# Kernel tuning notes

Hardware: AMD Instinct MI355X
Metric: run time of the kernel (lower is better)

The kernel has to match this reference:

```python
import jax, jax.numpy as jnp
import numpy as np

N = 200000
E = 600000
H = 128
OUT = 256
NUM_TYPES = 300
B = 128


def setup_inputs() -> dict:
    key = jax.random.key(0)
    ks = jax.random.split(key, 12)
    x = jax.random.randint(ks[0], (N,), 0, NUM_TYPES)
    edge_index = jax.random.randint(ks[1], (2, E), 0, N)
    batch = jnp.sort(jax.random.randint(ks[2], (N,), 0, B))
    s = 1.0 / np.sqrt(H)
    emb = jax.random.normal(ks[3], (NUM_TYPES, H), jnp.float32)
    W0 = jax.random.uniform(ks[4], (H, H), jnp.float32, -s, s)
    b0 = jax.random.uniform(ks[5], (H,), jnp.float32, -s, s)
    W1 = jax.random.uniform(ks[6], (H, H), jnp.float32, -s, s)
    b1 = jax.random.uniform(ks[7], (H,), jnp.float32, -s, s)
    Wo = jax.random.uniform(ks[8], (H, OUT), jnp.float32, -s, s)
    bo = jax.random.uniform(ks[9], (OUT,), jnp.float32, -s, s)
    gamma = jnp.ones((OUT,), jnp.float32)
    beta = jnp.zeros((OUT,), jnp.float32)
    return {"x": x, "edge_index": edge_index, "batch": batch, "batch_size": B,
            "emb": emb, "W0": W0, "b0": b0, "W1": W1, "b1": b1,
            "Wo": Wo, "bo": bo, "gamma": gamma, "beta": beta}


def gcn_layer(h, full_src, full_dst, W, b, n):
    # gather messages, scatter-add to destinations (bidirectional edges pre-built)
    msg = h[full_src]                                   # [2E, H]
    agg = jax.ops.segment_sum(msg, full_dst, num_segments=n)
    deg = jax.ops.segment_sum(jnp.ones((full_src.shape[0],), h.dtype),
                              full_dst, num_segments=n)
    deg = jnp.sqrt(jnp.clip(deg, 1.0))[:, None]
    out = agg / deg
    out = out @ W + b
    out = out + h
    return jax.nn.gelu(out, approximate=False)  # torch nn.GELU default is exact


def reference(x, edge_index, batch, batch_size, emb, W0, b0, W1, b1, Wo, bo, gamma, beta):
    n = x.shape[0]
    h = emb[x]                                          # [N, H] embedding gather
    src, dst = edge_index[0], edge_index[1]
    full_src = jnp.concatenate([src, dst])
    full_dst = jnp.concatenate([dst, src])
    h = gcn_layer(h, full_src, full_dst, W0, b0, n)
    h = gcn_layer(h, full_src, full_dst, W1, b1, n)
    # segment-mean pooling per graph
    gsum = jax.ops.segment_sum(h, batch, num_segments=batch_size)
    cnt = jax.ops.segment_sum(jnp.ones((n,), h.dtype), batch, num_segments=batch_size)
    gfeat = gsum / jnp.clip(cnt, 1.0)[:, None]
    out = gfeat @ Wo + bo
    mu = jnp.mean(out, axis=-1, keepdims=True)
    var = jnp.var(out, axis=-1, keepdims=True)
    out = (out - mu) * jax.lax.rsqrt(var + 1e-5) * gamma + beta
    return out
```

## Files before the change

### kernel.cpp

```cpp
#include <hip/hip_runtime.h>
#include <hip/hip_bf16.h>
#include <hip/hip_fp8.h>
#include <math.h>

#define H 128
#define OUTD 256
#define ASTRIDE 40
#define NODE_MASK 0x3FFFF

typedef unsigned short ushort_t;
typedef unsigned int uint_t;
typedef unsigned char uchar_t;
typedef __attribute__((ext_vector_type(8))) short short8;
typedef __attribute__((ext_vector_type(4))) float f32x4;
typedef __attribute__((ext_vector_type(2))) float f32x2;

__device__ __forceinline__ float bf2f(uint_t u){
    union { uint_t i; float f; } v; v.i = u << 16; return v.f;
}
__device__ __forceinline__ uint_t f2bf(float f){
    __hip_bfloat16 b = __float2bfloat16(f);
    union { __hip_bfloat16 b; ushort_t u; } v; v.b = b; return (uint_t)v.u;
}
__device__ __forceinline__ float fp8tof(uint_t u){
    __hip_fp8_e4m3 t; t.__x = (__hip_fp8_storage_t)u; return (float)t;
}
__device__ __forceinline__ uint_t ftofp8(float f){
    __hip_fp8_e4m3 t(f); return (uint_t)t.__x;
}
__device__ __forceinline__ uint_t pk2fp8(float a, float b){
#if __has_builtin(__builtin_amdgcn_cvt_pk_fp8_f32)
    return (uint_t)__builtin_amdgcn_cvt_pk_fp8_f32(a, b, 0, false) & 0xFFFFu;
#else
    return ftofp8(a) | (ftofp8(b) << 8);
#endif
}
__device__ __forceinline__ void acc_fp8(f32x4& v, uint_t u){
#if __has_builtin(__builtin_amdgcn_cvt_pk_f32_fp8)
    f32x2 lo = __builtin_amdgcn_cvt_pk_f32_fp8(u, false);
    f32x2 hi = __builtin_amdgcn_cvt_pk_f32_fp8(u, true);
    f32x2 a = {v[0], v[1]}, b2 = {v[2], v[3]};
    a += lo; b2 += hi;
    v = (f32x4){a[0], a[1], b2[0], b2[1]};
#else
    v[0] += fp8tof(u & 0xFFu);         v[1] += fp8tof((u >> 8) & 0xFFu);
    v[2] += fp8tof((u >> 16) & 0xFFu); v[3] += fp8tof(u >> 24);
#endif
}
__device__ __forceinline__ float gelu_fast(float x){
    float a = fabsf(x) * 0.70710678118654752440f;
    float t = __builtin_amdgcn_rcpf(fmaf(0.3275911f, a, 1.0f));
    float p = t*fmaf(t, fmaf(t, fmaf(t, fmaf(t, 1.061405429f, -1.453152027f),
                                     1.421413741f), -0.284496736f), 0.254829592f);
    float erf = 1.0f - p*__expf(-a*a);
    erf = copysignf(erf, x);
    return 0.5f * x * (1.0f + erf);
}

__global__ __launch_bounds__(256) void sniff_kernel(const ushort_t* __restrict__ data,
                                                    int count, int* __restrict__ flag_fp32){
    __shared__ float red[256];
    float m = 0.f;
    for (int i = threadIdx.x; i < count; i += 256){
        float v = fabsf(bf2f((uint_t)data[i]));
        if (isfinite(v)) m = fmaxf(m, v);
        else m = 1e30f;
    }
    red[threadIdx.x] = m;
    __syncthreads();
    #pragma unroll
    for (int s = 128; s > 0; s >>= 1){
        if (threadIdx.x < s) red[threadIdx.x] = fmaxf(red[threadIdx.x], red[threadIdx.x+s]);
        __syncthreads();
    }
    if (threadIdx.x == 0) *flag_fp32 = (red[0] > 100.f) ? 1 : 0;
}

struct StageArgs {
    const void* src[7];
    float*      dst[7];
    int         count[7];
    int         blk_off[8];
};
__global__ __launch_bounds__(256) void stage_all_kernel(StageArgs args,
                                                        const int* __restrict__ flag_fp32){
    int bx = blockIdx.x;
    int seg = 0;
    while (seg < 6 && bx >= args.blk_off[seg+1]) seg++;
    int idx = (bx - args.blk_off[seg])*256 + threadIdx.x;
    if (idx >= args.count[seg]) return;
    const int isf32 = *flag_fp32;
    args.dst[seg][idx] = isf32 ? ((const float*)args.src[seg])[idx]
                               : bf2f((uint_t)((const ushort_t*)args.src[seg])[idx]);
}

__global__ __launch_bounds__(256) void transpose_w_kernel(
        const void* __restrict__ Ws0, const void* __restrict__ Ws1,
        const void* __restrict__ embsrc, int szEmb,
        ushort_t* __restrict__ d0, ushort_t* __restrict__ d1,
        ushort_t* __restrict__ dEmb, uchar_t* __restrict__ dEmb8,
        int* __restrict__ zero_base, int zero_count,
        const int* __restrict__ flag_fp32){
    if (blockIdx.y == 3){
        for (int i = blockIdx.x*256 + threadIdx.x; i < zero_count; i += gridDim.x*256)
            zero_base[i] = 0;
        return;
    }
    const int isf32 = *flag_fp32;
    if (blockIdx.y == 2){
        int i = blockIdx.x*256 + threadIdx.x;
        if (i >= szEmb) return;
        ushort_t bv = isf32 ? (ushort_t)f2bf(((const float*)embsrc)[i])
                            : ((const ushort_t*)embsrc)[i];
        dEmb[i] = bv;
        int row = i >> 7, col = i & 127;
        int kb = col >> 5, qq = (col >> 3) & 3, jj = col & 7;
        dEmb8[(size_t)row*H + qq*32 + kb*8 + jj] = (uchar_t)ftofp8(bf2f((uint_t)bv));
        return;
    }
    const void* s = blockIdx.y ? Ws1 : Ws0;
    ushort_t*   d = blockIdx.y ? d1  : d0;
    int i = blockIdx.x*256 + threadIdx.x;
    if (i >= H*H) return;
    int k = i >> 7, nn = i & 127;
    ushort_t v = isf32 ? (ushort_t)f2bf(((const float*)s)[i])
                       : ((const ushort_t*)s)[i];
    d[nn*H + k] = v;
}

__global__ __launch_bounds__(256) void fill_part_kernel(const int* __restrict__ src,
        const int* __restrict__ dst, const int* __restrict__ x,
        int* __restrict__ deg, int* __restrict__ adj, int E, int n){
    int group = blockIdx.x & 7;
    int gblk  = blockIdx.x >> 3;
    int G     = gridDim.x >> 3;
    int lo = (int)(((long long)n * group) / 8);
    int hi = (int)(((long long)n * (group+1)) / 8);
    for (int e = gblk*256 + threadIdx.x; e < E; e += G*256){
        int s = src[e], d = dst[e];
        if (d >= lo && d < hi){
            int ts = x[s];
            int p = atomicAdd(&deg[d], 1);
            if (p < ASTRIDE) adj[(size_t)d*ASTRIDE + p] = s | (ts << 18);
        }
        if (s >= lo && s < hi){
            int td = x[d];
            int p = atomicAdd(&deg[s], 1);
            if (p < ASTRIDE) adj[(size_t)s*ASTRIDE + p] = d | (td << 18);
        }
    }
}

__global__ __launch_bounds__(512, 6) void gcn_fused(
    const int* __restrict__ deg, const int* __restrict__ adj,
    const ushort_t* __restrict__ gsrc, const uchar_t* __restrict__ g8,
    const int* __restrict__ xmap,
    const ushort_t* __restrict__ WT, const float* __restrict__ b,
    ushort_t* __restrict__ h_out, uchar_t* __restrict__ h8_out,
    int n, int use_x){
    __shared__ ushort_t Wt[128*136];
    for (int i = threadIdx.x; i < 2048; i += 512){
        int nn = i >> 4;
        int k0 = (i & 15) << 3;
        *(uint4*)(&Wt[nn*136 + k0]) = *(const uint4*)(WT + nn*H + k0);
    }
    __syncthreads();
    const int lane = threadIdx.x & 63;
    const int wave = threadIdx.x >> 6;
    const int quad = lane >> 4;
    const int lid  = lane & 15;

    int row = blockIdx.x*128 + wave*16 + lid;
    int cnt = (row < n) ? deg[row] : 0;
    float s = rsqrtf((float)(cnt < 1 ? 1 : cnt));
    if (cnt > ASTRIDE) cnt = ASTRIDE;
    const uint_t* ap = (const uint_t*)(adj + (size_t)row*ASTRIDE);

    f32x4 g[8];
    #pragma unroll
    for (int i=0;i<8;i++) g[i] = (f32x4){0.f,0.f,0.f,0.f};

    uint4 c0 = {0,0,0,0}, c1 = {0,0,0,0}, n0 = {0,0,0,0}, n1 = {0,0,0,0};
    if (cnt > 0){
        uint_t e = ap[0];
        size_t ro = (size_t)(use_x ? (e >> 18) : (e & NODE_MASK)) * H;
        const uchar_t* hp = g8 + ro + quad*32;
        c0 = *(const uint4*)(hp); c1 = *(const uint4*)(hp + 16);
    }
    if (cnt > 1){
        uint_t e = ap[1];
        size_t ro = (size_t)(use_x ? (e >> 18) : (e & NODE_MASK)) * H;
        const uchar_t* hp = g8 + ro + quad*32;
        n0 = *(const uint4*)(hp); n1 = *(const uint4*)(hp + 16);
    }
    for (int j=0; j<cnt; j++){
        uint4 f0 = {0,0,0,0}, f1 = {0,0,0,0};
        if (j+2 < cnt){
            uint_t e = ap[j+2];
            size_t ro = (size_t)(use_x ? (e >> 18) : (e & NODE_MASK)) * H;
            const uchar_t* hp = g8 + ro + quad*32;
            f0 = *(const uint4*)(hp); f1 = *(const uint4*)(hp + 16);
        }
        acc_fp8(g[0], c0.x); acc_fp8(g[1], c0.y);
        acc_fp8(g[2], c0.z); acc_fp8(g[3], c0.w);
        acc_fp8(g[4], c1.x); acc_fp8(g[5], c1.y);
        acc_fp8(g[6], c1.z); acc_fp8(g[7], c1.w);
        c0 = n0; c1 = n1; n0 = f0; n1 = f1;
    }

    short8 afrag[4];
    #pragma unroll
    for (int kb=0;kb<4;kb++){
        uint_t w0 = f2bf(g[2*kb][0]*s)   | (f2bf(g[2*kb][1]*s)   << 16);
        uint_t w1 = f2bf(g[2*kb][2]*s)   | (f2bf(g[2*kb][3]*s)   << 16);
        uint_t w2 = f2bf(g[2*kb+1][0]*s) | (f2bf(g[2*kb+1][1]*s) << 16);
        uint_t w3 = f2bf(g[2*kb+1][2]*s) | (f2bf(g[2*kb+1][3]*s) << 16);
        uint4 packed; packed.x=w0; packed.y=w1; packed.z=w2; packed.w=w3;
        afrag[kb] = *(short8*)&packed;
    }

    f32x4 acc[8];
    #pragma unroll
    for (int ct=0;ct<8;ct++) acc[ct] = (f32x4){0.f,0.f,0.f,0.f};
    #pragma unroll
    for (int kb=0;kb<4;kb++){
        #pragma unroll
        for (int ct=0;ct<8;ct++){
            short8 bf = *(const short8*)(&Wt[(ct*16+lid)*136 + kb*32 + quad*8]);
            acc[ct] = __builtin_amdgcn_mfma_f32_16x16x32_bf16(afrag[kb], bf, acc[ct], 0,0,0);
        }
    }

    float bcol[8];
    #pragma unroll
    for (int ct=0;ct<8;ct++) bcol[ct] = b[ct*16 + lid];
    int rowq = blockIdx.x*128 + wave*16 + quad*4;
    bool full = (blockIdx.x*128 + wave*16 + 16) <= n;
    const int boff = ((lid >> 3) << 5) + (lid & 7);
    #pragma unroll
    for (int r=0;r<4;r++){
        int grow = rowq + r;
        if (full || grow < n){
            if (use_x){
                const ushort_t* hr = gsrc + (size_t)xmap[grow]*H + lid;
                uchar_t* o8 = h8_out + (size_t)grow*H;
                float vv[8];
                #pragma unroll
                for (int ct=0;ct<8;ct++){
                    float hv = bf2f((uint_t)hr[ct*16]);
                    vv[ct] = gelu_fast(acc[ct][r] + bcol[ct] + hv);
                }
                #pragma unroll
                for (int cp=0;cp<4;cp++){
                    uint_t pk = pk2fp8(vv[2*cp], vv[2*cp+1]);
                    o8[boff + cp*8]      = (uchar_t)(pk & 0xFF);
                    o8[boff + 64 + cp*8] = (uchar_t)(pk >> 8);
                }
            } else {
                const uchar_t* h8r = g8 + (size_t)grow*H;
                ushort_t* orp = h_out + (size_t)grow*H + lid;
                #pragma unroll
                for (int ct=0;ct<8;ct++){
                    int off2 = boff + ((ct & 1) << 6) + ((ct >> 1) << 3);
                    float hv = fp8tof((uint_t)h8r[off2]);
                    float v  = gelu_fast(acc[ct][r] + bcol[ct] + hv);
                    orp[ct*16] = (ushort_t)f2bf(v);
                }
            }
        }
    }
}

__global__ __launch_bounds__(256) void pool_kernel(const ushort_t* __restrict__ h,
        const int* __restrict__ batch, float* __restrict__ gfeat, int n){
    int g = blockIdx.x;
    int q = blockIdx.y;
    __shared__ int se[2];
    if (threadIdx.x == 0){
        int lo=0, hi=n;
        while (lo<hi){ int m=(lo+hi)>>1; if (batch[m] < g) lo=m+1; else hi=m; }
        se[0] = lo;
        hi = n;
        while (lo<hi){ int m=(lo+hi)>>1; if (batch[m] <= g) lo=m+1; else hi=m; }
        se[1] = lo;
    }
    __syncthreads();
    int start = se[0], end = se[1];
    int chunk = (end - start + 3) >> 2;
    int s = start + q*chunk;
    int e = s + chunk; if (e > end) e = end;
    int col0 = (threadIdx.x & 15) << 3;
    int rg   = threadIdx.x >> 4;
    float acc[8];
    #pragma unroll
    for (int i=0;i<8;i++) acc[i] = 0.f;
    for (int r = s + rg; r < e; r += 16){
        uint4 raw = *(const uint4*)(h + (size_t)r*H + col0);
        acc[0] += bf2f(raw.x & 0xFFFFu); acc[1] += bf2f(raw.x >> 16);
        acc[2] += bf2f(raw.y & 0xFFFFu); acc[3] += bf2f(raw.y >> 16);
        acc[4] += bf2f(raw.z & 0xFFFFu); acc[5] += bf2f(raw.z >> 16);
        acc[6] += bf2f(raw.w & 0xFFFFu); acc[7] += bf2f(raw.w >> 16);
    }
    __shared__ float red[16][128];
    #pragma unroll
    for (int i=0;i<8;i++) red[rg][col0+i] = acc[i];
    __syncthreads();
    #pragma unroll
    for (int st=8; st>=1; st>>=1){
        if (rg < st){
            #pragma unroll
            for (int i=0;i<8;i++) red[rg][col0+i] += red[rg+st][col0+i];
        }
        __syncthreads();
    }
    if (rg == 0){
        #pragma unroll
        for (int i=0;i<8;i++) atomicAdd(&gfeat[(size_t)g*H + col0 + i], red[0][col0+i]);
    }
}

__global__ __launch_bounds__(256) void head_kernel(const float* __restrict__ gfeat,
        const int* __restrict__ batch, int n,
        const float* __restrict__ Wo, const float* __restrict__ bo,
        const float* __restrict__ gamma, const float* __restrict__ beta,
        void* __restrict__ out, const int* __restrict__ flag_fp32){
    int g = blockIdx.x;
    int j = threadIdx.x;
    __shared__ float gf[H];
    __shared__ float icnt_sh;
    if (j == 0){
        int lo=0, hi=n;
        while (lo<hi){ int m=(lo+hi)>>1; if (batch[m] < g) lo=m+1; else hi=m; }
        int st = lo;
        hi = n;
        while (lo<hi){ int m=(lo+hi)>>1; if (batch[m] <= g) lo=m+1; else hi=m; }
        int cnt = lo - st; if (cnt < 1) cnt = 1;
        icnt_sh = 1.0f / (float)cnt;
    }
    __syncthreads();
    if (j < H) gf[j] = gfeat[(size_t)g*H + j] * icnt_sh;
    __syncthreads();
    float acc = bo[j];
    #pragma unroll 8
    for (int k=0;k<H;k++) acc += gf[k] * Wo[(size_t)k*OUTD + j];
    __shared__ float red[256];
    red[j] = acc;
    __syncthreads();
    #pragma unroll
    for (int s2=128;s2>0;s2>>=1){
        if (j < s2) red[j] += red[j+s2];
        __syncthreads();
    }
    float mu = red[0] * (1.f/OUTD);
    __syncthreads();
    float d = acc - mu;
    red[j] = d*d;
    __syncthreads();
    #pragma unroll
    for (int s2=128;s2>0;s2>>=1){
        if (j < s2) red[j] += red[j+s2];
        __syncthreads();
    }
    float var = red[0] * (1.f/OUTD);
    float val = d * rsqrtf(var + 1e-5f) * gamma[j] + beta[j];
    size_t idx = (size_t)g*OUTD + j;
    if (*flag_fp32) ((float*)out)[idx] = val;
    else            ((ushort_t*)out)[idx] = (ushort_t)f2bf(val);
}

extern "C" void kernel_launch(void* const* d_in, const int* in_sizes, int n_in,
                              void* d_out, int out_size, void* d_ws, size_t ws_size,
                              hipStream_t stream){
    const int* x     = (const int*)d_in[0];
    const int* edge  = (const int*)d_in[1];
    const int* batch = (const int*)d_in[2];

    const int n = in_sizes[0];
    const int E = in_sizes[1] / 2;
    const int B = out_size / OUTD;
    const int* srcp = edge;
    const int* dstp = edge + E;

    const int szEmb = in_sizes[4], szb0 = in_sizes[6], szb1 = in_sizes[8];
    const int szWo = in_sizes[9], szbo = in_sizes[10], szg = in_sizes[11], szbt = in_sizes[12];

    char* base = (char*)d_ws;
    size_t off = 0;
    auto take = [&](size_t bytes)->char*{
        char* p = base + off;
        off = (off + bytes + 15) & ~(size_t)15;
        return p;
    };
    int*   flag   = (int*)  take(4);
    ushort_t* embb= (ushort_t*)take((size_t)szEmb*2);
    uchar_t* emb8 = (uchar_t*)take((size_t)szEmb);
    ushort_t* WT0 = (ushort_t*)take((size_t)H*H*2);
    ushort_t* WT1 = (ushort_t*)take((size_t)H*H*2);
    float* sb0    = (float*)take((size_t)szb0*4);
    float* sb1    = (float*)take((size_t)szb1*4);
    float* sWo    = (float*)take((size_t)szWo*4);
    float* sbo    = (float*)take((size_t)szbo*4);
    float* sg     = (float*)take((size_t)szg*4);
    float* sbt    = (float*)take((size_t)szbt*4);
    int*   adj    = (int*)  take((size_t)n*ASTRIDE*4);
    ushort_t* hA  = (ushort_t*)take((size_t)n*H*2);
    uchar_t*  h8  = (uchar_t*)take((size_t)n*H);
    char* zbase   = take((size_t)n*4 + (size_t)B*H*4);
    int*   deg    = (int*)zbase;
    float* gfeat  = (float*)(zbase + (size_t)n*4);
    const int zero_ints = n + B*H;

    sniff_kernel<<<1, 256, 0, stream>>>((const ushort_t*)d_in[4], szEmb, flag);

    StageArgs sa;
    const void* ssrc[7] = {d_in[9], d_in[6], d_in[8], d_in[10], d_in[11], d_in[12], d_in[10]};
    float*      sdst[7] = {sWo, sb0, sb1, sbo, sg, sbt, sbo};
    int         scnt[7] = {szWo, szb0, szb1, szbo, szg, szbt, 0};
    int run = 0;
    for (int i=0;i<7;i++){
        sa.src[i] = ssrc[i]; sa.dst[i] = sdst[i]; sa.count[i] = scnt[i];
        sa.blk_off[i] = run; run += (scnt[i] + 255)/256;
    }
    sa.blk_off[7] = run;
    stage_all_kernel<<<run, 256, 0, stream>>>(sa, flag);
    int tgrid = ((H*H > szEmb ? H*H : szEmb) + 255)/256;
    transpose_w_kernel<<<dim3(tgrid, 4), 256, 0, stream>>>(d_in[5], d_in[7],
                                                           d_in[4], szEmb,
                                                           WT0, WT1, embb, emb8,
                                                           (int*)zbase, zero_ints, flag);

    fill_part_kernel<<<2048, 256, 0, stream>>>(srcp, dstp, x, deg, adj, E, n);

    const int nblk = (n + 127) / 128;
    gcn_fused<<<nblk, 512, 0, stream>>>(deg, adj, embb, emb8, x,
                                        WT0, sb0, (ushort_t*)nullptr, h8, n, 1);
    gcn_fused<<<nblk, 512, 0, stream>>>(deg, adj, embb, h8, x,
                                        WT1, sb1, hA, (uchar_t*)nullptr, n, 0);

    pool_kernel<<<dim3(B,4), 256, 0, stream>>>(hA, batch, gfeat, n);
    head_kernel<<<B, 256, 0, stream>>>(gfeat, batch, n, sWo, sbo, sg, sbt, d_out, flag);
}
```

Measured before the change: 353.8 us.

## Cache fp8 embedding table in LDS for layer-one gather and parallelize sniff

The first GCN layer gathers neighbor features directly from the embedding table (indexed by node type). This change stages the whole fp8 table (300x128) into LDS with a padded stride, so neighbor gathers become LDS reads instead of global loads. The first 12 adjacency entries are fetched as vector loads and the gather is unrolled. The input-format sniff reduction is split across 64 blocks plus a finalize kernel. The larger LDS footprint (about 34KB extra per block) may lower occupancy under the 512-thread launch bounds, and the extra kernel launch adds overhead.

```diff
diff --git a/kernel.cpp b/kernel.cpp
--- a/kernel.cpp
+++ b/kernel.cpp
@@ -7,6 +7,8 @@
 #define OUTD 256
 #define ASTRIDE 40
 #define NODE_MASK 0x3FFFF
+#define EPAD 144
+#define EMB_LDS_MAX 38400
 
 typedef unsigned short ushort_t;
 typedef unsigned int uint_t;
@@ -57,11 +59,11 @@
     return 0.5f * x * (1.0f + erf);
 }
 
-__global__ __launch_bounds__(256) void sniff_kernel(const ushort_t* __restrict__ data,
-                                                    int count, int* __restrict__ flag_fp32){
+__global__ __launch_bounds__(256) void sniff_part(const ushort_t* __restrict__ data,
+                                                  int count, float* __restrict__ partial){
     __shared__ float red[256];
     float m = 0.f;
-    for (int i = threadIdx.x; i < count; i += 256){
+    for (int i = blockIdx.x*256 + threadIdx.x; i < count; i += gridDim.x*256){
         float v = fabsf(bf2f((uint_t)data[i]));
         if (isfinite(v)) m = fmaxf(m, v);
         else m = 1e30f;
@@ -73,7 +75,15 @@
         if (threadIdx.x < s) red[threadIdx.x] = fmaxf(red[threadIdx.x], red[threadIdx.x+s]);
         __syncthreads();
     }
-    if (threadIdx.x == 0) *flag_fp32 = (red[0] > 100.f) ? 1 : 0;
+    if (threadIdx.x == 0) partial[blockIdx.x] = red[0];
+}
+__global__ __launch_bounds__(64) void sniff_fin(const float* __restrict__ partial,
+                                                int nb, int* __restrict__ flag_fp32){
+    if (threadIdx.x == 0){
+        float m = 0.f;
+        for (int i = 0; i < nb; i++) m = fmaxf(m, partial[i]);
+        *flag_fp32 = (m > 100.f) ? 1 : 0;
+    }
 }
 
 struct StageArgs {
@@ -151,18 +161,38 @@
     }
 }
 
+#define L1STEP(EV) do { if (jcur < cnt){ \
+    uint_t t_ = (EV) >> 18; \
+    const uchar_t* hp_ = &Es[t_*EPAD + quad*32]; \
+    uint4 r0_ = *(const uint4*)(hp_); \
+    uint4 r1_ = *(const uint4*)(hp_ + 16); \
+    acc_fp8(g[0], r0_.x); acc_fp8(g[1], r0_.y); \
+    acc_fp8(g[2], r0_.z); acc_fp8(g[3], r0_.w); \
+    acc_fp8(g[4], r1_.x); acc_fp8(g[5], r1_.y); \
+    acc_fp8(g[6], r1_.z); acc_fp8(g[7], r1_.w); } jcur++; } while(0)
+
+template<int MODE>
 __global__ __launch_bounds__(512, 6) void gcn_fused(
     const int* __restrict__ deg, const int* __restrict__ adj,
     const ushort_t* __restrict__ gsrc, const uchar_t* __restrict__ g8,
     const int* __restrict__ xmap,
     const ushort_t* __restrict__ WT, const float* __restrict__ b,
     ushort_t* __restrict__ h_out, uchar_t* __restrict__ h8_out,
-    int n, int use_x){
+    int n, int szEmb){
     __shared__ ushort_t Wt[128*136];
+    __shared__ uchar_t Es[(MODE == 1) ? 300*EPAD : 16];
     for (int i = threadIdx.x; i < 2048; i += 512){
         int nn = i >> 4;
         int k0 = (i & 15) << 3;
         *(uint4*)(&Wt[nn*136 + k0]) = *(const uint4*)(WT + nn*H + k0);
+    }
+    if (MODE == 1){
+        const uint4* esrc = (const uint4*)g8;
+        int nq = szEmb >> 4;
+        for (int i = threadIdx.x; i < nq; i += 512){
+            int r = i >> 3, c = i & 7;
+            *(uint4*)(&Es[r*EPAD + c*16]) = esrc[i];
+        }
     }
     __syncthreads();
     const int lane = threadIdx.x & 63;
@@ -180,32 +210,52 @@
     #pragma unroll
     for (int i=0;i<8;i++) g[i] = (f32x4){0.f,0.f,0.f,0.f};
 
-    uint4 c0 = {0,0,0,0}, c1 = {0,0,0,0}, n0 = {0,0,0,0}, n1 = {0,0,0,0};
-    if (cnt > 0){
-        uint_t e = ap[0];
-        size_t ro = (size_t)(use_x ? (e >> 18) : (e & NODE_MASK)) * H;
-        const uchar_t* hp = g8 + ro + quad*32;
-        c0 = *(const uint4*)(hp); c1 = *(const uint4*)(hp + 16);
-    }
-    if (cnt > 1){
-        uint_t e = ap[1];
-        size_t ro = (size_t)(use_x ? (e >> 18) : (e & NODE_MASK)) * H;
-        const uchar_t* hp = g8 + ro + quad*32;
-        n0 = *(const uint4*)(hp); n1 = *(const uint4*)(hp + 16);
-    }
-    for (int j=0; j<cnt; j++){
-        uint4 f0 = {0,0,0,0}, f1 = {0,0,0,0};
-        if (j+2 < cnt){
-            uint_t e = ap[j+2];
-            size_t ro = (size_t)(use_x ? (e >> 18) : (e & NODE_MASK)) * H;
+    if (MODE == 1){
+        const uint4* ap4 = (const uint4*)ap;
+        uint4 ew0 = {0,0,0,0}, ew1 = {0,0,0,0}, ew2 = {0,0,0,0};
+        if (row < n){ ew0 = ap4[0]; ew1 = ap4[1]; ew2 = ap4[2]; }
+        int jcur = 0;
+        L1STEP(ew0.x); L1STEP(ew0.y); L1STEP(ew0.z); L1STEP(ew0.w);
+        L1STEP(ew1.x); L1STEP(ew1.y); L1STEP(ew1.z); L1STEP(ew1.w);
+        L1STEP(ew2.x); L1STEP(ew2.y); L1STEP(ew2.z); L1STEP(ew2.w);
+        for (int j = 12; j < cnt; j++){
+            uint_t t = ap[j] >> 18;
+            const uchar_t* hp = &Es[t*EPAD + quad*32];
+            uint4 r0 = *(const uint4*)(hp);
+            uint4 r1 = *(const uint4*)(hp + 16);
+            acc_fp8(g[0], r0.x); acc_fp8(g[1], r0.y);
+            acc_fp8(g[2], r0.z); acc_fp8(g[3], r0.w);
+            acc_fp8(g[4], r1.x); acc_fp8(g[5], r1.y);
+            acc_fp8(g[6], r1.z); acc_fp8(g[7], r1.w);
+        }
+    } else {
+        uint4 c0 = {0,0,0,0}, c1 = {0,0,0,0}, n0 = {0,0,0,0}, n1 = {0,0,0,0};
+        if (cnt > 0){
+            uint_t e = ap[0];
+            size_t ro = (size_t)(MODE ? (e >> 18) : (e & NODE_MASK)) * H;
             const uchar_t* hp = g8 + ro + quad*32;
-            f0 = *(const uint4*)(hp); f1 = *(const uint4*)(hp + 16);
-        }
-        acc_fp8(g[0], c0.x); acc_fp8(g[1], c0.y);
-        acc_fp8(g[2], c0.z); acc_fp8(g[3], c0.w);
-        acc_fp8(g[4], c1.x); acc_fp8(g[5], c1.y);
-        acc_fp8(g[6], c1.z); acc_fp8(g[7], c1.w);
-        c0 = n0; c1 = n1; n0 = f0; n1 = f1;
+            c0 = *(const uint4*)(hp); c1 = *(const uint4*)(hp + 16);
+        }
+        if (cnt > 1){
+            uint_t e = ap[1];
+            size_t ro = (size_t)(MODE ? (e >> 18) : (e & NODE_MASK)) * H;
+            const uchar_t* hp = g8 + ro + quad*32;
+            n0 = *(const uint4*)(hp); n1 = *(const uint4*)(hp + 16);
+        }
+        for (int j=0; j<cnt; j++){
+            uint4 f0 = {0,0,0,0}, f1 = {0,0,0,0};
+            if (j+2 < cnt){
+                uint_t e = ap[j+2];
+                size_t ro = (size_t)(MODE ? (e >> 18) : (e & NODE_MASK)) * H;
+                const uchar_t* hp = g8 + ro + quad*32;
+                f0 = *(const uint4*)(hp); f1 = *(const uint4*)(hp + 16);
+            }
+            acc_fp8(g[0], c0.x); acc_fp8(g[1], c0.y);
+            acc_fp8(g[2], c0.z); acc_fp8(g[3], c0.w);
+            acc_fp8(g[4], c1.x); acc_fp8(g[5], c1.y);
+            acc_fp8(g[6], c1.z); acc_fp8(g[7], c1.w);
+            c0 = n0; c1 = n1; n0 = f0; n1 = f1;
+        }
     }
 
     short8 afrag[4];
@@ -241,7 +291,7 @@
     for (int r=0;r<4;r++){
         int grow = rowq + r;
         if (full || grow < n){
-            if (use_x){
+            if (MODE != 0){
                 const ushort_t* hr = gsrc + (size_t)xmap[grow]*H + lid;
                 uchar_t* o8 = h8_out + (size_t)grow*H;
                 float vv[8];
@@ -392,6 +442,7 @@
         return p;
     };
     int*   flag   = (int*)  take(4);
+    float* spart  = (float*)take(64*4);
     ushort_t* embb= (ushort_t*)take((size_t)szEmb*2);
     uchar_t* emb8 = (uchar_t*)take((size_t)szEmb);
     ushort_t* WT0 = (ushort_t*)take((size_t)H*H*2);
@@ -410,7 +461,8 @@
     float* gfeat  = (float*)(zbase + (size_t)n*4);
     const int zero_ints = n + B*H;
 
-    sniff_kernel<<<1, 256, 0, stream>>>((const ushort_t*)d_in[4], szEmb, flag);
+    sniff_part<<<64, 256, 0, stream>>>((const ushort_t*)d_in[4], szEmb, spart);
+    sniff_fin<<<1, 64, 0, stream>>>(spart, 64, flag);
 
     StageArgs sa;
     const void* ssrc[7] = {d_in[9], d_in[6], d_in[8], d_in[10], d_in[11], d_in[12], d_in[10]};
@@ -432,10 +484,17 @@
     fill_part_kernel<<<2048, 256, 0, stream>>>(srcp, dstp, x, deg, adj, E, n);
 
     const int nblk = (n + 127) / 128;
-    gcn_fused<<<nblk, 512, 0, stream>>>(deg, adj, embb, emb8, x,
-                                        WT0, sb0, (ushort_t*)nullptr, h8, n, 1);
-    gcn_fused<<<nblk, 512, 0, stream>>>(deg, adj, embb, h8, x,
-                                        WT1, sb1, hA, (uchar_t*)nullptr, n, 0);
+    if (szEmb <= EMB_LDS_MAX)
+        gcn_fused<1><<<nblk, 512, 0, stream>>>(deg, adj, embb, emb8, x,
+                                               WT0, sb0, (ushort_t*)nullptr, h8,
+                                               n, szEmb);
+    else
+        gcn_fused<2><<<nblk, 512, 0, stream>>>(deg, adj, embb, emb8, x,
+                                               WT0, sb0, (ushort_t*)nullptr, h8,
+                                               n, szEmb);
+    gcn_fused<0><<<nblk, 512, 0, stream>>>(deg, adj, embb, h8, x,
+                                           WT1, sb1, hA, (uchar_t*)nullptr,
+                                           n, szEmb);
 
     pool_kernel<<<dim3(B,4), 256, 0, stream>>>(hA, batch, gfeat, n);
     head_kernel<<<B, 256, 0, stream>>>(gfeat, batch, n, sWo, sbo, sg, sbt, d_out, flag);
```

Result: faster. 301.1 us (-14.9%).
